# Kernel optimization log

Measured on AMD Instinct MI355X. Metric: run time of the kernel, lower is better.

## Reference

```python
import jax, jax.numpy as jnp
import numpy as np
from jax import lax

B, L, D, N, R, NC = 8, 1024, 1024, 16, 64, 1000  # batch, seq, d_inner, d_state, dt_rank, num_classes


def setup_inputs() -> dict:
    key = jax.random.key(0)
    ks = jax.random.split(key, 6)
    x = jax.random.normal(ks[0], (B, L, D), dtype=jnp.float32)
    # Mamba S4D-real init: A = 1..N broadcast over channels, stored as log
    A_log = jnp.log(jnp.broadcast_to(jnp.arange(1, N + 1, dtype=jnp.float32), (D, N)))
    D_param = jnp.ones((D,), dtype=jnp.float32)
    W_xproj = jax.random.normal(ks[1], (R + 2 * N, D), dtype=jnp.float32) * 0.02
    W_dt = jax.random.normal(ks[2], (D, R), dtype=jnp.float32) * 0.02
    b_dt = jax.random.normal(ks[3], (D,), dtype=jnp.float32) * 0.02
    W_cls = jax.random.normal(ks[4], (NC, D), dtype=jnp.float32) * 0.02
    b_cls = jnp.zeros((NC,), dtype=jnp.float32)
    return {"x": x, "A_log": A_log, "D_param": D_param, "W_xproj": W_xproj,
            "W_dt": W_dt, "b_dt": b_dt, "W_cls": W_cls, "b_cls": b_cls}


def reference(x, A_log, D_param, W_xproj, W_dt, b_dt, W_cls, b_cls):
    # x: [B, L, D] -> project to dt_rank + 2*d_state (no bias, as in Mamba)
    xdb = jnp.einsum('bld,kd->blk', x, W_xproj)          # [B, L, R+2N]
    dt_r = xdb[..., :R]                                   # [B, L, R]
    Bm = xdb[..., R:R + N]                                # [B, L, N]
    Cm = xdb[..., R + N:]                                 # [B, L, N]
    # softplus on dt
    dt = jax.nn.softplus(jnp.einsum('blr,dr->bld', dt_r, W_dt) + b_dt)  # [B, L, D]
    # discretization
    A = -jnp.exp(A_log)                                   # [D, N]
    dA = jnp.exp(dt[..., None] * A)                       # [B, L, D, N]
    dBx = dt[..., None] * Bm[:, :, None, :] * x[..., None]  # [B, L, D, N]

    # sequential scan over time
    def step(h, inp):
        dA_t, dBx_t, C_t = inp                            # [B,D,N],[B,D,N],[B,N]
        h = dA_t * h + dBx_t
        y = jnp.einsum('bdn,bn->bd', h, C_t)
        return h, y

    h0 = jnp.zeros((B, D, N), dtype=x.dtype)
    _, ys = lax.scan(step, h0, (jnp.moveaxis(dA, 1, 0),
                                jnp.moveaxis(dBx, 1, 0),
                                jnp.moveaxis(Cm, 1, 0)))   # ys: [L, B, D]
    y = jnp.moveaxis(ys, 0, 1) + D_param * x              # [B, L, D] skip term

    pooled = y.mean(axis=1)                               # AdaptiveAvgPool1d(1) over L
    logits = pooled @ W_cls.T + b_cls                     # [B, NC]
    return logits
```

## Files before the change

### kernel.cpp

```cpp
#include <hip/hip_runtime.h>
#include <hip/hip_bf16.h>

#define B_  8
#define L_  1024
#define D_  1024
#define N_  16
#define R_  64
#define NC_ 1000

#define XP_KS   8
#define XP_TM   64
#define XP_KC   (D_ / XP_KS)
#define XP_M    (B_ * L_)

#define CH8  8
#define TCH8 (L_ / CH8)
#define TB   32

__global__ __launch_bounds__(256) void xproj_kernel(
    const float* __restrict__ x, const float* __restrict__ W,
    float* __restrict__ part) {
  __shared__ float xs[XP_TM][36];
  __shared__ float wt[32][100];
  const int tid = threadIdx.x;
  const int tx = tid & 7;
  const int ty = tid >> 3;
  const int m0 = blockIdx.x * XP_TM;
  const int ks = blockIdx.y;

  float acc[2][12];
#pragma unroll
  for (int r = 0; r < 2; ++r)
#pragma unroll
    for (int j = 0; j < 12; ++j) acc[r][j] = 0.f;

  for (int step = 0; step < XP_KC / 32; ++step) {
    const int kbase = ks * XP_KC + step * 32;
    __syncthreads();
#pragma unroll
    for (int j = 0; j < 2; ++j) {
      const int f4 = tid + j * 256;
      const int row = f4 >> 3, c4 = f4 & 7;
      float4 v = *(const float4*)(x + (size_t)(m0 + row) * D_ + kbase + c4 * 4);
      *(float4*)(&xs[row][c4 * 4]) = v;
    }
#pragma unroll
    for (int j = 0; j < 3; ++j) {
      const int idx = tid + j * 256;
      const int wr = idx >> 3, c4 = idx & 7;
      float4 v = *(const float4*)(W + (size_t)wr * D_ + kbase + c4 * 4);
      wt[c4 * 4 + 0][wr] = v.x;
      wt[c4 * 4 + 1][wr] = v.y;
      wt[c4 * 4 + 2][wr] = v.z;
      wt[c4 * 4 + 3][wr] = v.w;
    }
    __syncthreads();
#pragma unroll 4
    for (int kk = 0; kk < 32; ++kk) {
      const float a0 = xs[ty * 2 + 0][kk];
      const float a1 = xs[ty * 2 + 1][kk];
      const float4 b0 = *(const float4*)(&wt[kk][tx * 12 + 0]);
      const float4 b1 = *(const float4*)(&wt[kk][tx * 12 + 4]);
      const float4 b2 = *(const float4*)(&wt[kk][tx * 12 + 8]);
      acc[0][0] = fmaf(a0, b0.x, acc[0][0]);
      acc[0][1] = fmaf(a0, b0.y, acc[0][1]);
      acc[0][2] = fmaf(a0, b0.z, acc[0][2]);
      acc[0][3] = fmaf(a0, b0.w, acc[0][3]);
      acc[0][4] = fmaf(a0, b1.x, acc[0][4]);
      acc[0][5] = fmaf(a0, b1.y, acc[0][5]);
      acc[0][6] = fmaf(a0, b1.z, acc[0][6]);
      acc[0][7] = fmaf(a0, b1.w, acc[0][7]);
      acc[0][8] = fmaf(a0, b2.x, acc[0][8]);
      acc[0][9] = fmaf(a0, b2.y, acc[0][9]);
      acc[0][10] = fmaf(a0, b2.z, acc[0][10]);
      acc[0][11] = fmaf(a0, b2.w, acc[0][11]);
      acc[1][0] = fmaf(a1, b0.x, acc[1][0]);
      acc[1][1] = fmaf(a1, b0.y, acc[1][1]);
      acc[1][2] = fmaf(a1, b0.z, acc[1][2]);
      acc[1][3] = fmaf(a1, b0.w, acc[1][3]);
      acc[1][4] = fmaf(a1, b1.x, acc[1][4]);
      acc[1][5] = fmaf(a1, b1.y, acc[1][5]);
      acc[1][6] = fmaf(a1, b1.z, acc[1][6]);
      acc[1][7] = fmaf(a1, b1.w, acc[1][7]);
      acc[1][8] = fmaf(a1, b2.x, acc[1][8]);
      acc[1][9] = fmaf(a1, b2.y, acc[1][9]);
      acc[1][10] = fmaf(a1, b2.z, acc[1][10]);
      acc[1][11] = fmaf(a1, b2.w, acc[1][11]);
    }
  }
#pragma unroll
  for (int r = 0; r < 2; ++r) {
    float* p = part + ((size_t)ks * XP_M + m0 + ty * 2 + r) * 96 + tx * 12;
    *(float4*)(p + 0) = make_float4(acc[r][0], acc[r][1], acc[r][2], acc[r][3]);
    *(float4*)(p + 4) = make_float4(acc[r][4], acc[r][5], acc[r][6], acc[r][7]);
    *(float4*)(p + 8) = make_float4(acc[r][8], acc[r][9], acc[r][10], acc[r][11]);
  }
}

__global__ __launch_bounds__(256) void xreduce_kernel(
    const float* __restrict__ part, float* __restrict__ xdb) {
  const size_t gidx = (size_t)blockIdx.x * 256 + threadIdx.x;
  const float4* p4 = (const float4*)part;
  const size_t stride = (size_t)XP_M * 96 / 4;
  float4 s = p4[gidx];
#pragma unroll
  for (int ks = 1; ks < XP_KS; ++ks) {
    const float4 v = p4[(size_t)ks * stride + gidx];
    s.x += v.x; s.y += v.y; s.z += v.z; s.w += v.w;
  }
  ((float4*)xdb)[gidx] = s;
}

__global__ __launch_bounds__(256, 4) void dt_kernel(
    const float* __restrict__ xdb, const float* __restrict__ W_dt,
    const float* __restrict__ b_dt, float* __restrict__ dtb) {
  __shared__ float dtr[16][64];
  const int tid = threadIdx.x;
  const int d = blockIdx.y * 256 + tid;
  const int m0 = blockIdx.x * 16;

  float4 w[16];
#pragma unroll
  for (int i = 0; i < 16; ++i)
    w[i] = *(const float4*)(W_dt + (size_t)d * R_ + i * 4);
  const float bd = b_dt[d];

  {
    const int row = tid >> 4, c4 = tid & 15;
    *(float4*)(&dtr[row][c4 * 4]) =
        *(const float4*)(xdb + (size_t)(m0 + row) * 96 + c4 * 4);
  }
  __syncthreads();

#pragma unroll 4
  for (int row = 0; row < 16; ++row) {
    float a0 = 0.f, a1 = 0.f, a2 = 0.f, a3 = 0.f;
#pragma unroll
    for (int rc = 0; rc < 16; ++rc) {
      const float4 v = *(const float4*)(&dtr[row][rc * 4]);
      a0 = fmaf(v.x, w[rc].x, a0);
      a1 = fmaf(v.y, w[rc].y, a1);
      a2 = fmaf(v.z, w[rc].z, a2);
      a3 = fmaf(v.w, w[rc].w, a3);
    }
    const float s = bd + ((a0 + a1) + (a2 + a3));
    const float sp = fmaxf(s, 0.f) + __logf(1.0f + __expf(-fabsf(s)));
    dtb[(size_t)(m0 + row) * D_ + d] = sp;
  }
}

__global__ __launch_bounds__(256) void scan_kernel(
    const float* __restrict__ x, const float* __restrict__ xdb,
    const float* __restrict__ dtb, const float* __restrict__ A_log,
    float* __restrict__ summ, float* __restrict__ sumx) {
  __shared__ float xs[TB][32];
  __shared__ float dts[TB][32];
  __shared__ float bcs[TB][32];
  const int tid = threadIdx.x;
  const int n = tid & 15;
  const int dl = tid >> 4;
  const int b = blockIdx.x >> 5;
  const int dtile = blockIdx.x & 31;
  const int c = blockIdx.y;
  const int d0 = dtile * 32;
  const int da = d0 + dl, db = d0 + dl + 16;

  const float Av0 = -__expf(A_log[(size_t)da * N_ + n]);
  const float Av1 = -__expf(A_log[(size_t)db * N_ + n]);

  const int t0 = c * TCH8;
  float cumP0 = 1.f, loc0 = 0.f, S10 = 0.f, S20 = 0.f, xsum0 = 0.f;
  float cumP1 = 1.f, loc1 = 0.f, S11 = 0.f, S21 = 0.f, xsum1 = 0.f;

  const int srow = tid >> 3, sc4 = (tid & 7) * 4;

  for (int tb = 0; tb < TCH8; tb += TB) {
    const int tbase = t0 + tb;
    __syncthreads();
    {
      const size_t gx = ((size_t)b * L_ + tbase + srow) * D_ + d0 + sc4;
      *(float4*)(&xs[srow][sc4]) = *(const float4*)(x + gx);
      *(float4*)(&dts[srow][sc4]) = *(const float4*)(dtb + gx);
      const size_t gb = ((size_t)b * L_ + tbase + srow) * 96 + 64 + sc4;
      *(float4*)(&bcs[srow][sc4]) = *(const float4*)(xdb + gb);
    }
    __syncthreads();
#pragma unroll 8
    for (int tt = 0; tt < TB; ++tt) {
      const float Bv = bcs[tt][n];
      const float Cv = bcs[tt][16 + n];
      const float xv0 = xs[tt][dl];
      const float xv1 = xs[tt][dl + 16];
      const float dtv0 = dts[tt][dl];
      const float dtv1 = dts[tt][dl + 16];
      const float e0 = __expf(dtv0 * Av0);
      cumP0 *= e0;
      loc0 = fmaf(e0, loc0, dtv0 * Bv * xv0);
      S10 = fmaf(cumP0, Cv, S10);
      S20 = fmaf(loc0, Cv, S20);
      xsum0 += xv0;
      const float e1 = __expf(dtv1 * Av1);
      cumP1 *= e1;
      loc1 = fmaf(e1, loc1, dtv1 * Bv * xv1);
      S11 = fmaf(cumP1, Cv, S11);
      S21 = fmaf(loc1, Cv, S21);
      xsum1 += xv1;
    }
  }
  const size_t si0 = (((size_t)c * B_ + b) * D_ + da) * N_ + n;
  const size_t si1 = (((size_t)c * B_ + b) * D_ + db) * N_ + n;
  ((float4*)summ)[si0] = make_float4(cumP0, S10, S20, loc0);
  ((float4*)summ)[si1] = make_float4(cumP1, S11, S21, loc1);
  if (n == 0) {
    sumx[((size_t)c * B_ + b) * D_ + da] = xsum0;
    sumx[((size_t)c * B_ + b) * D_ + db] = xsum1;
  }
}

__global__ __launch_bounds__(256) void combine_kernel(
    const float* __restrict__ summ, const float* __restrict__ sumx,
    const float* __restrict__ D_param, float* __restrict__ pooled) {
  const int gid = blockIdx.x * 256 + threadIdx.x;
  const int n = gid & 15;
  const int d = (gid >> 4) & (D_ - 1);
  const int b = gid >> 14;
  float hin = 0.f, acc = 0.f;
  const float4* s4 = (const float4*)summ;
#pragma unroll
  for (int c = 0; c < CH8; ++c) {
    const float4 f = s4[(((size_t)c * B_ + b) * D_ + d) * N_ + n];
    acc = fmaf(hin, f.y, acc) + f.z;
    hin = fmaf(f.x, hin, f.w);
  }
  acc += __shfl_xor(acc, 1);
  acc += __shfl_xor(acc, 2);
  acc += __shfl_xor(acc, 4);
  acc += __shfl_xor(acc, 8);
  if (n == 0) {
    float xst = 0.f;
#pragma unroll
    for (int c = 0; c < CH8; ++c)
      xst += sumx[((size_t)c * B_ + b) * D_ + d];
    pooled[(size_t)b * D_ + d] =
        (acc + D_param[d] * xst) * (1.0f / (float)L_);
  }
}

__global__ __launch_bounds__(256) void cls_kernel(
    const float* __restrict__ pooled, const float* __restrict__ W_cls,
    const float* __restrict__ b_cls, float* __restrict__ out) {
  __shared__ float pool[B_ * D_];
  const int tid = threadIdx.x;
  const int c = blockIdx.x * 4 + (tid >> 6);
  const int lane = tid & 63;

#pragma unroll
  for (int j = 0; j < 8; ++j) {
    const int f4 = tid + j * 256;
    ((float4*)pool)[f4] = ((const float4*)pooled)[f4];
  }
  __syncthreads();

  float accb[B_];
#pragma unroll
  for (int b = 0; b < B_; ++b) accb[b] = 0.f;

#pragma unroll
  for (int i = 0; i < 4; ++i) {
    const float4 wv =
        *(const float4*)(W_cls + (size_t)c * D_ + i * 256 + lane * 4);
#pragma unroll
    for (int b = 0; b < B_; ++b) {
      const float4 p = *(const float4*)(&pool[b * D_ + i * 256 + lane * 4]);
      accb[b] = fmaf(wv.x, p.x,
                fmaf(wv.y, p.y, fmaf(wv.z, p.z, fmaf(wv.w, p.w, accb[b]))));
    }
  }
#pragma unroll
  for (int off = 1; off < 64; off <<= 1) {
#pragma unroll
    for (int b = 0; b < B_; ++b) accb[b] += __shfl_xor(accb[b], off);
  }
  if (lane < B_) out[(size_t)lane * NC_ + c] = accb[lane] + b_cls[c];
}

extern "C" void kernel_launch(void* const* d_in, const int* in_sizes, int n_in,
                              void* d_out, int out_size, void* d_ws,
                              size_t ws_size, hipStream_t stream) {
  const float* x = (const float*)d_in[0];
  const float* A_log = (const float*)d_in[1];
  const float* D_param = (const float*)d_in[2];
  const float* W_xproj = (const float*)d_in[3];
  const float* W_dt = (const float*)d_in[4];
  const float* b_dt = (const float*)d_in[5];
  const float* W_cls = (const float*)d_in[6];
  const float* b_cls = (const float*)d_in[7];
  float* out = (float*)d_out;

  float* ws_f = (float*)d_ws;
  float* xdb = ws_f;
  float* part = xdb + (size_t)XP_M * 96;
  float* dtb = part + (size_t)XP_KS * XP_M * 96;
  float* summ = dtb + (size_t)XP_M * D_;
  float* sumx = summ + (size_t)CH8 * B_ * D_ * N_ * 4;
  float* pooled = sumx + (size_t)CH8 * B_ * D_;

  xproj_kernel<<<dim3(XP_M / XP_TM, XP_KS), dim3(256), 0, stream>>>(
      x, W_xproj, part);
  xreduce_kernel<<<dim3(XP_M * 96 / 4 / 256), dim3(256), 0, stream>>>(part,
                                                                      xdb);
  dt_kernel<<<dim3(XP_M / 16, 4), dim3(256), 0, stream>>>(xdb, W_dt, b_dt,
                                                          dtb);
  scan_kernel<<<dim3(B_ * 32, CH8), dim3(256), 0, stream>>>(x, xdb, dtb,
                                                            A_log, summ, sumx);
  combine_kernel<<<dim3(B_ * D_ * N_ / 256), dim3(256), 0, stream>>>(
      summ, sumx, D_param, pooled);
  cls_kernel<<<dim3(NC_ / 4), dim3(256), 0, stream>>>(pooled, W_cls, b_cls,
                                                      out);
}
```

Baseline: 124.5 us.

## Streamline scan inner loop with exp2, premultiplied dt*x, and paired LDS reads

```diff
diff --git a/kernel.cpp b/kernel.cpp
--- a/kernel.cpp
+++ b/kernel.cpp
@@ -16,6 +16,16 @@
 #define CH8  8
 #define TCH8 (L_ / CH8)
 #define TB   32
+
+__device__ __forceinline__ float exp2_fast(float a) {
+#if __has_builtin(__builtin_amdgcn_exp2f)
+  return __builtin_amdgcn_exp2f(a);
+#else
+  float r;
+  asm("v_exp_f32 %0, %1" : "=v"(r) : "v"(a));
+  return r;
+#endif
+}
 
 __global__ __launch_bounds__(256) void xproj_kernel(
     const float* __restrict__ x, const float* __restrict__ W,
@@ -153,9 +163,9 @@
     const float* __restrict__ x, const float* __restrict__ xdb,
     const float* __restrict__ dtb, const float* __restrict__ A_log,
     float* __restrict__ summ, float* __restrict__ sumx) {
-  __shared__ float xs[TB][32];
   __shared__ float dts[TB][32];
-  __shared__ float bcs[TB][32];
+  __shared__ float dtx[TB][32];
+  __shared__ float bcs[TB][34];
   const int tid = threadIdx.x;
   const int n = tid & 15;
   const int dl = tid >> 4;
@@ -163,57 +173,68 @@
   const int dtile = blockIdx.x & 31;
   const int c = blockIdx.y;
   const int d0 = dtile * 32;
-  const int da = d0 + dl, db = d0 + dl + 16;
-
-  const float Av0 = -__expf(A_log[(size_t)da * N_ + n]);
-  const float Av1 = -__expf(A_log[(size_t)db * N_ + n]);
+  const int da = d0 + 2 * dl, db = da + 1;
+
+  const float Av0 = -__expf(A_log[(size_t)da * N_ + n]) * 1.44269504089f;
+  const float Av1 = -__expf(A_log[(size_t)db * N_ + n]) * 1.44269504089f;
 
   const int t0 = c * TCH8;
-  float cumP0 = 1.f, loc0 = 0.f, S10 = 0.f, S20 = 0.f, xsum0 = 0.f;
-  float cumP1 = 1.f, loc1 = 0.f, S11 = 0.f, S21 = 0.f, xsum1 = 0.f;
+  float cumP0 = 1.f, loc0 = 0.f, S10 = 0.f, S20 = 0.f;
+  float cumP1 = 1.f, loc1 = 0.f, S11 = 0.f, S21 = 0.f;
+  float xp0 = 0.f, xp1 = 0.f, xp2 = 0.f, xp3 = 0.f;
 
   const int srow = tid >> 3, sc4 = (tid & 7) * 4;
+  const int bpos = ((sc4 * 2) & 31) + (sc4 >> 4);
 
   for (int tb = 0; tb < TCH8; tb += TB) {
     const int tbase = t0 + tb;
     __syncthreads();
     {
-      const size_t gx = ((size_t)b * L_ + tbase + srow) * D_ + d0 + sc4;
-      *(float4*)(&xs[srow][sc4]) = *(const float4*)(x + gx);
-      *(float4*)(&dts[srow][sc4]) = *(const float4*)(dtb + gx);
+      const size_t g = ((size_t)b * L_ + tbase + srow) * D_ + d0 + sc4;
+      const float4 xv = *(const float4*)(x + g);
+      const float4 dv = *(const float4*)(dtb + g);
+      *(float4*)(&dts[srow][sc4]) = dv;
+      *(float4*)(&dtx[srow][sc4]) =
+          make_float4(xv.x * dv.x, xv.y * dv.y, xv.z * dv.z, xv.w * dv.w);
+      xp0 += xv.x; xp1 += xv.y; xp2 += xv.z; xp3 += xv.w;
       const size_t gb = ((size_t)b * L_ + tbase + srow) * 96 + 64 + sc4;
-      *(float4*)(&bcs[srow][sc4]) = *(const float4*)(xdb + gb);
+      const float4 bc = *(const float4*)(xdb + gb);
+      bcs[srow][bpos + 0] = bc.x;
+      bcs[srow][bpos + 2] = bc.y;
+      bcs[srow][bpos + 4] = bc.z;
+      bcs[srow][bpos + 6] = bc.w;
     }
     __syncthreads();
-#pragma unroll 8
+#pragma unroll
     for (int tt = 0; tt < TB; ++tt) {
-      const float Bv = bcs[tt][n];
-      const float Cv = bcs[tt][16 + n];
-      const float xv0 = xs[tt][dl];
-      const float xv1 = xs[tt][dl + 16];
-      const float dtv0 = dts[tt][dl];
-      const float dtv1 = dts[tt][dl + 16];
-      const float e0 = __expf(dtv0 * Av0);
+      const float2 bv = *(const float2*)(&bcs[tt][2 * n]);
+      const float2 dv = *(const float2*)(&dts[tt][2 * dl]);
+      const float2 px = *(const float2*)(&dtx[tt][2 * dl]);
+      const float e0 = exp2_fast(dv.x * Av0);
       cumP0 *= e0;
-      loc0 = fmaf(e0, loc0, dtv0 * Bv * xv0);
-      S10 = fmaf(cumP0, Cv, S10);
-      S20 = fmaf(loc0, Cv, S20);
-      xsum0 += xv0;
-      const float e1 = __expf(dtv1 * Av1);
+      loc0 = fmaf(e0, loc0, px.x * bv.x);
+      S10 = fmaf(cumP0, bv.y, S10);
+      S20 = fmaf(loc0, bv.y, S20);
+      const float e1 = exp2_fast(dv.y * Av1);
       cumP1 *= e1;
-      loc1 = fmaf(e1, loc1, dtv1 * Bv * xv1);
-      S11 = fmaf(cumP1, Cv, S11);
-      S21 = fmaf(loc1, Cv, S21);
-      xsum1 += xv1;
+      loc1 = fmaf(e1, loc1, px.y * bv.x);
+      S11 = fmaf(cumP1, bv.y, S11);
+      S21 = fmaf(loc1, bv.y, S21);
     }
   }
   const size_t si0 = (((size_t)c * B_ + b) * D_ + da) * N_ + n;
   const size_t si1 = (((size_t)c * B_ + b) * D_ + db) * N_ + n;
   ((float4*)summ)[si0] = make_float4(cumP0, S10, S20, loc0);
   ((float4*)summ)[si1] = make_float4(cumP1, S11, S21, loc1);
-  if (n == 0) {
-    sumx[((size_t)c * B_ + b) * D_ + da] = xsum0;
-    sumx[((size_t)c * B_ + b) * D_ + db] = xsum1;
+
+  __syncthreads();
+  *(float4*)(&dtx[srow][sc4]) = make_float4(xp0, xp1, xp2, xp3);
+  __syncthreads();
+  if (tid < 32) {
+    float s = 0.f;
+#pragma unroll
+    for (int r = 0; r < 32; ++r) s += dtx[r][tid];
+    sumx[((size_t)c * B_ + b) * D_ + d0 + tid] = s;
   }
 }
 
```

Result: faster. 114.4 us (-8.1%).
